# Kernel optimization log

Hardware: AMD Instinct MI355X
Metric: run time of the kernel (lower is better)

## Reference

```python
import jax, jax.numpy as jnp
import numpy as np


def setup_inputs() -> dict:
    key = jax.random.key(0)
    k1, k2, k3, k4, k5 = jax.random.split(key, 5)
    B, N, M, D = 16, 8192, 8192, 256
    emb = jax.random.normal(k1, (B, M, D), dtype=jnp.float32)
    pts = jax.random.normal(k2, (B, N, 5), dtype=jnp.float32)
    num = jax.random.randint(k3, (B,), 1, M + 1)
    indeces = jax.random.randint(k4, (B, M), 0, N)
    W = jax.random.normal(k5, (4, D), dtype=jnp.float32) * (1.414 / np.sqrt(4 + D))
    image_shape = jnp.array([B, 3, 768, 1024], dtype=jnp.int64)  # (b, c, H, W)
    return {"emb": emb, "num": num, "pts": pts, "indeces": indeces,
            "image_shape": image_shape, "W": W}


def reference(emb, num, pts, indeces, image_shape, W):
    height = image_shape[2].astype(jnp.float32)
    width = image_shape[3].astype(jnp.float32)
    # normalize_keypoints: center at image center, scale by 0.7*max(W,H)
    size = jnp.stack([width, height])                      # [2] (w, h)
    center = size / 2.0
    scaling = jnp.max(size) * 0.7
    upts = (pts[..., :2] - center) / scaling               # [B,N,2]
    # normalize_angle: (angle - 45) / (180*0.7)
    uangle = (pts[..., 4:5] - 45.0) / (180.0 * 0.7)        # [B,N,1]
    # normalize_len: scale by 0.7*diag, center at half that
    diag = jnp.sqrt(width * width + height * height)
    lscale = diag * 0.7
    ulen = (pts[..., 3:4] - lscale / 2.0) / lscale         # [B,N,1]
    feat = jnp.concatenate([upts, uangle, ulen], axis=-1)  # [B,N,4]
    pose_feature = jnp.einsum("bnf,fd->bnd", feat, W)      # [B,N,D]
    # per-batch gather of pose_feature rows, added to first num[b] emb slots
    gathered = jnp.take_along_axis(pose_feature, indeces[..., None], axis=1)  # [B,M,D]
    slot = jnp.arange(emb.shape[1])[None, :]               # [1,M]
    mask = (slot < num[:, None])[..., None]                # [B,M,1]
    return emb + jnp.where(mask, gathered, 0.0)
```

## Files before the change

### kernel.cpp

```cpp
#include <hip/hip_runtime.h>


typedef float f32x4 __attribute__((ext_vector_type(4)));

#define DD 256

__global__ __launch_bounds__(256) void posfeat_d256_kernel(
    const float* __restrict__ emb,
    const int* __restrict__ num,
    const float* __restrict__ pts,
    const int* __restrict__ indeces,
    const int* __restrict__ image_shape,
    const float* __restrict__ W,
    float* __restrict__ out,
    int B, int M, int N, int tiles_per_b, int total_tiles)
{
    const int lane = threadIdx.x & 63;
    const int wave = threadIdx.x >> 6;
    const int waves_per_grid = gridDim.x * 4;

    const float h = (float)image_shape[2];
    const float w = (float)image_shape[3];
    const float inv_s  = 1.0f / (fmaxf(w, h) * 0.7f);
    const float cx = w * 0.5f, cy = h * 0.5f;
    const float lscale = sqrtf(w * w + h * h) * 0.7f;
    const float inv_l  = 1.0f / lscale;
    const float half_l = lscale * 0.5f;
    const float inv_a  = 1.0f / 126.0f;

    const int d0 = lane * 4;
    const f32x4 w0 = *(const f32x4*)(W + 0 * DD + d0);
    const f32x4 w1 = *(const f32x4*)(W + 1 * DD + d0);
    const f32x4 w2 = *(const f32x4*)(W + 2 * DD + d0);
    const f32x4 w3 = *(const f32x4*)(W + 3 * DD + d0);

    const int pr = lane / 5, pc = lane - pr * 5;

    for (int tile = blockIdx.x * 4 + wave; tile < total_tiles; tile += waves_per_grid) {
        const int b      = tile / tiles_per_b;
        const int base_m = (tile - b * tiles_per_b) * 8;
        const int nb     = num[b];

        int idxv = -1;
        if (lane < 8) {
            const int m = base_m + lane;
            if (m < M && m < nb) idxv = indeces[(long long)b * M + m];
        }
        const int ir_g = __shfl(idxv, pr);
        float pv = 0.f;
        if (lane < 40 && ir_g >= 0)
            pv = pts[((long long)b * N + ir_g) * 5 + pc];

        const long long baseoff = ((long long)b * M + base_m) * DD + d0;
        const int nrows = (M - base_m < 8) ? (M - base_m) : 8;

        f32x4 e[8];
        #pragma unroll
        for (int r = 0; r < 8; ++r)
            if (r < nrows) e[r] = *(const f32x4*)(emb + baseoff + (long long)r * DD);

        #pragma unroll
        for (int r = 0; r < 8; ++r) {
            if (r >= nrows) continue;
            const int   ir = __shfl(idxv, r);
            const float p0 = __shfl(pv, r * 5 + 0);
            const float p1 = __shfl(pv, r * 5 + 1);
            const float p3 = __shfl(pv, r * 5 + 3);
            const float p4 = __shfl(pv, r * 5 + 4);
            float f0 = 0.f, f1 = 0.f, f2 = 0.f, f3 = 0.f;
            if (ir >= 0) {
                f0 = (p0 - cx) * inv_s;
                f1 = (p1 - cy) * inv_s;
                f2 = (p4 - 45.0f) * inv_a;
                f3 = (p3 - half_l) * inv_l;
            }
            f32x4 o;
            o.x = e[r].x + f0 * w0.x + f1 * w1.x + f2 * w2.x + f3 * w3.x;
            o.y = e[r].y + f0 * w0.y + f1 * w1.y + f2 * w2.y + f3 * w3.y;
            o.z = e[r].z + f0 * w0.z + f1 * w1.z + f2 * w2.z + f3 * w3.z;
            o.w = e[r].w + f0 * w0.w + f1 * w1.w + f2 * w2.w + f3 * w3.w;
            __builtin_nontemporal_store(o, (f32x4*)(out + baseoff + (long long)r * DD));
        }
    }
}

__global__ __launch_bounds__(256) void posfeat_generic_kernel(
    const float* __restrict__ emb, const int* __restrict__ num,
    const float* __restrict__ pts, const int* __restrict__ indeces,
    const int* __restrict__ image_shape, const float* __restrict__ W,
    float* __restrict__ out, int B, int M, int N, int D)
{
    const int lane = threadIdx.x & 63;
    const int wave = threadIdx.x >> 6;
    const int m = blockIdx.x * 4 + wave;
    const int b = blockIdx.y;
    if (m >= M) return;
    const float h = (float)image_shape[2];
    const float w = (float)image_shape[3];
    const float inv_s = 1.0f / (fmaxf(w, h) * 0.7f);
    const float cx = w * 0.5f, cy = h * 0.5f;
    const float lscale = sqrtf(w * w + h * h) * 0.7f;
    const float inv_l = 1.0f / lscale;
    const float inv_a = 1.0f / 126.0f;
    float f0 = 0.f, f1 = 0.f, f2 = 0.f, f3 = 0.f;
    if (m < num[b]) {
        const int idx = indeces[(long long)b * M + m];
        const float* p = pts + ((long long)b * N + (long long)idx) * 5;
        f0 = (p[0] - cx) * inv_s;
        f1 = (p[1] - cy) * inv_s;
        f2 = (p[4] - 45.0f) * inv_a;
        f3 = (p[3] - lscale * 0.5f) * inv_l;
    }
    const long long rowoff = ((long long)b * M + m) * (long long)D;
    for (int dd = lane * 4; dd < D; dd += 64 * 4) {
        const f32x4 w0 = *(const f32x4*)(W + 0 * D + dd);
        const f32x4 w1 = *(const f32x4*)(W + 1 * D + dd);
        const f32x4 w2 = *(const f32x4*)(W + 2 * D + dd);
        const f32x4 w3 = *(const f32x4*)(W + 3 * D + dd);
        const f32x4 e  = *(const f32x4*)(emb + rowoff + dd);
        f32x4 r;
        r.x = e.x + f0 * w0.x + f1 * w1.x + f2 * w2.x + f3 * w3.x;
        r.y = e.y + f0 * w0.y + f1 * w1.y + f2 * w2.y + f3 * w3.y;
        r.z = e.z + f0 * w0.z + f1 * w1.z + f2 * w2.z + f3 * w3.z;
        r.w = e.w + f0 * w0.w + f1 * w1.w + f2 * w2.w + f3 * w3.w;
        *(f32x4*)(out + rowoff + dd) = r;
    }
}

extern "C" void kernel_launch(void* const* d_in, const int* in_sizes, int n_in,
                              void* d_out, int out_size, void* d_ws, size_t ws_size,
                              hipStream_t stream) {
    (void)n_in; (void)d_ws; (void)ws_size; (void)out_size;
    const float* emb  = (const float*)d_in[0];
    const int*   num  = (const int*)d_in[1];
    const float* pts  = (const float*)d_in[2];
    const int*   idx  = (const int*)d_in[3];
    const int*   ishp = (const int*)d_in[4];
    const float* Wm   = (const float*)d_in[5];
    float*       out  = (float*)d_out;

    const int B = in_sizes[1];
    const int D = in_sizes[5] / 4;
    const int M = (int)((long long)in_sizes[3] / B);
    const int N = (int)((long long)in_sizes[2] / ((long long)B * 5));

    if (D == 256) {
        const int tiles_per_b = (M + 7) / 8;
        const int total_tiles = B * tiles_per_b;
        int blocks = (total_tiles + 3) / 4;
        if (blocks > 2048) blocks = 2048;
        hipLaunchKernelGGL(posfeat_d256_kernel, dim3(blocks), dim3(256), 0, stream,
                           emb, num, pts, idx, ishp, Wm, out, B, M, N,
                           tiles_per_b, total_tiles);
    } else {
        dim3 block(256);
        dim3 grid((M + 3) / 4, B);
        hipLaunchKernelGGL(posfeat_generic_kernel, grid, block, 0, stream,
                           emb, num, pts, idx, ishp, Wm, out, B, M, N, D);
    }
}
```

Before: 46.79 us.

## Prefetch next tile's index and point gather, use 2D grid per batch

The kernel now uses a 2D grid with one grid row per batch, so the batch index and num[b] are hoisted out of the tile loop. Each wave software-pipelines the dependent indeces→pts gather, fetching the next tile's indices and point values while the current tile's embedding rows are processed. The per-row bounds checks are dropped by requiring M divisible by 8, and other shapes fall back to the generic kernel. This targets the latency of the two chained gathers, at the cost of extra registers for the prefetched values.

Result: no change. 46.07 us (-1.5%).

```diff
diff --git a/kernel.cpp b/kernel.cpp
--- a/kernel.cpp
+++ b/kernel.cpp
@@ -13,11 +13,13 @@
     const int* __restrict__ image_shape,
     const float* __restrict__ W,
     float* __restrict__ out,
-    int B, int M, int N, int tiles_per_b, int total_tiles)
+    int M, int N, int tiles_per_b)
 {
     const int lane = threadIdx.x & 63;
     const int wave = threadIdx.x >> 6;
-    const int waves_per_grid = gridDim.x * 4;
+    const int b = blockIdx.y;
+    const int wv = blockIdx.x * 4 + wave;
+    const int stride = gridDim.x * 4;
 
     const float h = (float)image_shape[2];
     const float w = (float)image_shape[3];
@@ -35,38 +37,45 @@
     const f32x4 w3 = *(const f32x4*)(W + 3 * DD + d0);
 
     const int pr = lane / 5, pc = lane - pr * 5;
+    const int nb = num[b];
+    const long long embb = (long long)b * M;
+    const long long ptsb = (long long)b * N;
 
-    for (int tile = blockIdx.x * 4 + wave; tile < total_tiles; tile += waves_per_grid) {
-        const int b      = tile / tiles_per_b;
-        const int base_m = (tile - b * tiles_per_b) * 8;
-        const int nb     = num[b];
+    auto gather = [&](int tile, int& idxv, float& pv) {
+        idxv = -1;
+        if (lane < 8) {
+            const int m = tile * 8 + lane;
+            if (m < nb) idxv = indeces[embb + m];
+        }
+        const int ir = __shfl(idxv, pr);
+        pv = 0.f;
+        if (lane < 40 && ir >= 0)
+            pv = pts[(ptsb + ir) * 5 + pc];
+    };
 
-        int idxv = -1;
-        if (lane < 8) {
-            const int m = base_m + lane;
-            if (m < M && m < nb) idxv = indeces[(long long)b * M + m];
-        }
-        const int ir_g = __shfl(idxv, pr);
-        float pv = 0.f;
-        if (lane < 40 && ir_g >= 0)
-            pv = pts[((long long)b * N + ir_g) * 5 + pc];
+    int tile = wv;
+    int idx0 = -1; float pv0 = 0.f;
+    if (tile < tiles_per_b) gather(tile, idx0, pv0);
 
-        const long long baseoff = ((long long)b * M + base_m) * DD + d0;
-        const int nrows = (M - base_m < 8) ? (M - base_m) : 8;
+    for (; tile < tiles_per_b; tile += stride) {
+        const long long baseoff = (embb + (long long)tile * 8) * DD + d0;
 
         f32x4 e[8];
         #pragma unroll
         for (int r = 0; r < 8; ++r)
-            if (r < nrows) e[r] = *(const f32x4*)(emb + baseoff + (long long)r * DD);
+            e[r] = *(const f32x4*)(emb + baseoff + (long long)r * DD);
+
+        const int tile2 = tile + stride;
+        int idx1 = -1; float pv1 = 0.f;
+        if (tile2 < tiles_per_b) gather(tile2, idx1, pv1);
 
         #pragma unroll
         for (int r = 0; r < 8; ++r) {
-            if (r >= nrows) continue;
-            const int   ir = __shfl(idxv, r);
-            const float p0 = __shfl(pv, r * 5 + 0);
-            const float p1 = __shfl(pv, r * 5 + 1);
-            const float p3 = __shfl(pv, r * 5 + 3);
-            const float p4 = __shfl(pv, r * 5 + 4);
+            const int   ir = __shfl(idx0, r);
+            const float p0 = __shfl(pv0, r * 5 + 0);
+            const float p1 = __shfl(pv0, r * 5 + 1);
+            const float p3 = __shfl(pv0, r * 5 + 3);
+            const float p4 = __shfl(pv0, r * 5 + 4);
             float f0 = 0.f, f1 = 0.f, f2 = 0.f, f3 = 0.f;
             if (ir >= 0) {
                 f0 = (p0 - cx) * inv_s;
@@ -81,6 +90,7 @@
             o.w = e[r].w + f0 * w0.w + f1 * w1.w + f2 * w2.w + f3 * w3.w;
             __builtin_nontemporal_store(o, (f32x4*)(out + baseoff + (long long)r * DD));
         }
+        idx0 = idx1; pv0 = pv1;
     }
 }
 
@@ -144,14 +154,13 @@
     const int M = (int)((long long)in_sizes[3] / B);
     const int N = (int)((long long)in_sizes[2] / ((long long)B * 5));
 
-    if (D == 256) {
-        const int tiles_per_b = (M + 7) / 8;
-        const int total_tiles = B * tiles_per_b;
-        int blocks = (total_tiles + 3) / 4;
-        if (blocks > 2048) blocks = 2048;
-        hipLaunchKernelGGL(posfeat_d256_kernel, dim3(blocks), dim3(256), 0, stream,
-                           emb, num, pts, idx, ishp, Wm, out, B, M, N,
-                           tiles_per_b, total_tiles);
+    if (D == 256 && (M % 8) == 0) {
+        const int tiles_per_b = M / 8;
+        int bx = 2048 / B; if (bx < 1) bx = 1;
+        int waves_per_b = bx * 4;
+        if (waves_per_b > tiles_per_b) bx = (tiles_per_b + 3) / 4;
+        hipLaunchKernelGGL(posfeat_d256_kernel, dim3(bx, B), dim3(256), 0, stream,
+                           emb, num, pts, idx, ishp, Wm, out, M, N, tiles_per_b);
     } else {
         dim3 block(256);
         dim3 grid((M + 3) / 4, B);
```

## Split feature gather into separate kernel and stream emb with precomputed features

Applied to the files above, without the earlier changes.

The gather of pts rows and the keypoint normalization move into a first kernel that writes a per-row float4 feature buffer in the workspace. A second kernel then streams emb, loads the precomputed features, and applies the 4xD projection without shuffles or dependent gathers on the critical path. This is meant to take the latency of the dependent index-then-pts loads out of the bandwidth-bound streaming loop. In exchange it adds a second kernel launch and an extra workspace write and read of B*M*16 bytes. It also requires M divisible by 8 and enough workspace, otherwise it falls back to the generic kernel.

Result: slower. 49.72 us (+6.3%).

```diff
diff --git a/kernel.cpp b/kernel.cpp
--- a/kernel.cpp
+++ b/kernel.cpp
@@ -5,19 +5,18 @@
 
 #define DD 256
 
-__global__ __launch_bounds__(256) void posfeat_d256_kernel(
-    const float* __restrict__ emb,
+__global__ __launch_bounds__(256) void posfeat_feat_kernel(
     const int* __restrict__ num,
     const float* __restrict__ pts,
     const int* __restrict__ indeces,
     const int* __restrict__ image_shape,
-    const float* __restrict__ W,
-    float* __restrict__ out,
-    int B, int M, int N, int tiles_per_b, int total_tiles)
+    f32x4* __restrict__ feat,
+    int M, int N, int total)
 {
-    const int lane = threadIdx.x & 63;
-    const int wave = threadIdx.x >> 6;
-    const int waves_per_grid = gridDim.x * 4;
+    const int gid = blockIdx.x * 256 + threadIdx.x;
+    if (gid >= total) return;
+    const int b = gid / M;
+    const int m = gid - b * M;
 
     const float h = (float)image_shape[2];
     const float w = (float)image_shape[3];
@@ -28,58 +27,54 @@
     const float half_l = lscale * 0.5f;
     const float inv_a  = 1.0f / 126.0f;
 
+    f32x4 f = {0.f, 0.f, 0.f, 0.f};
+    if (m < num[b]) {
+        const int idx = indeces[gid];
+        const float* p = pts + ((long long)b * N + (long long)idx) * 5;
+        f.x = (p[0] - cx) * inv_s;
+        f.y = (p[1] - cy) * inv_s;
+        f.z = (p[4] - 45.0f) * inv_a;
+        f.w = (p[3] - half_l) * inv_l;
+    }
+    feat[gid] = f;
+}
+
+__global__ __launch_bounds__(256) void posfeat_stream_kernel(
+    const float* __restrict__ emb,
+    const f32x4* __restrict__ feat,
+    const float* __restrict__ W,
+    float* __restrict__ out,
+    int total_tiles)
+{
+    const int lane = threadIdx.x & 63;
+    const int wave = threadIdx.x >> 6;
+    const int stride = gridDim.x * 4;
     const int d0 = lane * 4;
+
     const f32x4 w0 = *(const f32x4*)(W + 0 * DD + d0);
     const f32x4 w1 = *(const f32x4*)(W + 1 * DD + d0);
     const f32x4 w2 = *(const f32x4*)(W + 2 * DD + d0);
     const f32x4 w3 = *(const f32x4*)(W + 3 * DD + d0);
 
-    const int pr = lane / 5, pc = lane - pr * 5;
+    for (int tile = blockIdx.x * 4 + wave; tile < total_tiles; tile += stride) {
+        const long long base = (long long)tile * 8;
 
-    for (int tile = blockIdx.x * 4 + wave; tile < total_tiles; tile += waves_per_grid) {
-        const int b      = tile / tiles_per_b;
-        const int base_m = (tile - b * tiles_per_b) * 8;
-        const int nb     = num[b];
-
-        int idxv = -1;
-        if (lane < 8) {
-            const int m = base_m + lane;
-            if (m < M && m < nb) idxv = indeces[(long long)b * M + m];
-        }
-        const int ir_g = __shfl(idxv, pr);
-        float pv = 0.f;
-        if (lane < 40 && ir_g >= 0)
-            pv = pts[((long long)b * N + ir_g) * 5 + pc];
-
-        const long long baseoff = ((long long)b * M + base_m) * DD + d0;
-        const int nrows = (M - base_m < 8) ? (M - base_m) : 8;
-
-        f32x4 e[8];
+        f32x4 e[8], f[8];
         #pragma unroll
         for (int r = 0; r < 8; ++r)
-            if (r < nrows) e[r] = *(const f32x4*)(emb + baseoff + (long long)r * DD);
+            e[r] = *(const f32x4*)(emb + (base + r) * DD + d0);
+        #pragma unroll
+        for (int r = 0; r < 8; ++r)
+            f[r] = feat[base + r];
 
         #pragma unroll
         for (int r = 0; r < 8; ++r) {
-            if (r >= nrows) continue;
-            const int   ir = __shfl(idxv, r);
-            const float p0 = __shfl(pv, r * 5 + 0);
-            const float p1 = __shfl(pv, r * 5 + 1);
-            const float p3 = __shfl(pv, r * 5 + 3);
-            const float p4 = __shfl(pv, r * 5 + 4);
-            float f0 = 0.f, f1 = 0.f, f2 = 0.f, f3 = 0.f;
-            if (ir >= 0) {
-                f0 = (p0 - cx) * inv_s;
-                f1 = (p1 - cy) * inv_s;
-                f2 = (p4 - 45.0f) * inv_a;
-                f3 = (p3 - half_l) * inv_l;
-            }
             f32x4 o;
-            o.x = e[r].x + f0 * w0.x + f1 * w1.x + f2 * w2.x + f3 * w3.x;
-            o.y = e[r].y + f0 * w0.y + f1 * w1.y + f2 * w2.y + f3 * w3.y;
-            o.z = e[r].z + f0 * w0.z + f1 * w1.z + f2 * w2.z + f3 * w3.z;
-            o.w = e[r].w + f0 * w0.w + f1 * w1.w + f2 * w2.w + f3 * w3.w;
-            __builtin_nontemporal_store(o, (f32x4*)(out + baseoff + (long long)r * DD));
+            o.x = e[r].x + f[r].x * w0.x + f[r].y * w1.x + f[r].z * w2.x + f[r].w * w3.x;
+            o.y = e[r].y + f[r].x * w0.y + f[r].y * w1.y + f[r].z * w2.y + f[r].w * w3.y;
+            o.z = e[r].z + f[r].x * w0.z + f[r].y * w1.z + f[r].z * w2.z + f[r].w * w3.z;
+            o.w = e[r].w + f[r].x * w0.w + f[r].y * w1.w + f[r].z * w2.w + f[r].w * w3.w;
+            __builtin_nontemporal_store(o, (f32x4*)(out + (base + r) * DD + d0));
         }
     }
 }
@@ -130,7 +125,7 @@
 extern "C" void kernel_launch(void* const* d_in, const int* in_sizes, int n_in,
                               void* d_out, int out_size, void* d_ws, size_t ws_size,
                               hipStream_t stream) {
-    (void)n_in; (void)d_ws; (void)ws_size; (void)out_size;
+    (void)n_in; (void)out_size;
     const float* emb  = (const float*)d_in[0];
     const int*   num  = (const int*)d_in[1];
     const float* pts  = (const float*)d_in[2];
@@ -144,14 +139,19 @@
     const int M = (int)((long long)in_sizes[3] / B);
     const int N = (int)((long long)in_sizes[2] / ((long long)B * 5));
 
-    if (D == 256) {
-        const int tiles_per_b = (M + 7) / 8;
-        const int total_tiles = B * tiles_per_b;
-        int blocks = (total_tiles + 3) / 4;
-        if (blocks > 2048) blocks = 2048;
-        hipLaunchKernelGGL(posfeat_d256_kernel, dim3(blocks), dim3(256), 0, stream,
-                           emb, num, pts, idx, ishp, Wm, out, B, M, N,
-                           tiles_per_b, total_tiles);
+    const int total = B * M;
+    const size_t ws_need = (size_t)total * sizeof(f32x4);
+
+    if (D == 256 && (M % 8) == 0 && ws_size >= ws_need) {
+        f32x4* feat = (f32x4*)d_ws;
+        const int blocks1 = (total + 255) / 256;
+        hipLaunchKernelGGL(posfeat_feat_kernel, dim3(blocks1), dim3(256), 0, stream,
+                           num, pts, idx, ishp, feat, M, N, total);
+        const int total_tiles = total / 8;
+        int blocks2 = (total_tiles + 3) / 4;
+        if (blocks2 > 2048) blocks2 = 2048;
+        hipLaunchKernelGGL(posfeat_stream_kernel, dim3(blocks2), dim3(256), 0, stream,
+                           emb, feat, Wm, out, total_tiles);
     } else {
         dim3 block(256);
         dim3 grid((M + 3) / 4, B);
```
